# Kernel tuning notes

Hardware: AMD Instinct MI355X
Metric: run time of the kernel (lower is better)

## Reference

```python
import jax, jax.numpy as jnp
import numpy as np

OUT = 7          # pooled output size
SR = 2           # sampling_ratio
STRIDES = (32, 16, 8, 4)          # coarse -> fine, matches feat0..feat3
ANCHORS = (512, 256, 128, 64)     # anchor sizes, large -> small


def _interp_1d(c, size):
    # torchvision roi_align bilinear edge handling (aligned=False)
    valid = (c >= -1.0) & (c <= size)
    cc = jnp.maximum(c, 0.0)
    lo_f = jnp.floor(cc)
    at_edge = lo_f >= size - 1
    lo = jnp.where(at_edge, size - 1.0, lo_f)
    hi = jnp.where(at_edge, size - 1.0, lo_f + 1.0)
    frac = jnp.where(at_edge, 0.0, cc - lo_f)
    return lo.astype(jnp.int32), hi.astype(jnp.int32), frac, valid


def _roi_align(feat, rois, scale):
    # feat: [B,C,H,W], rois: [N,5] = (batch_id, x1, y1, x2, y2)
    B, C, H, W = feat.shape
    N = rois.shape[0]
    b = rois[:, 0].astype(jnp.int32)
    x1, y1, x2, y2 = (rois[:, i] * scale for i in (1, 2, 3, 4))
    roi_w = jnp.maximum(x2 - x1, 1.0)
    roi_h = jnp.maximum(y2 - y1, 1.0)
    bin_h = roi_h / OUT
    bin_w = roi_w / OUT
    off = (jnp.arange(SR) + 0.5) / SR                                 # [SR]
    grid = (jnp.arange(OUT)[:, None] + off[None, :]).reshape(-1)      # [OUT*SR]
    ys = y1[:, None] + grid[None, :] * bin_h[:, None]                 # [N, OUT*SR]
    xs = x1[:, None] + grid[None, :] * bin_w[:, None]
    yl, yh, fy, vy = _interp_1d(ys, H)
    xl, xh, fx, vx = _interp_1d(xs, W)
    ft = jnp.transpose(feat, (0, 2, 3, 1))                            # [B,H,W,C]

    def g(yi, xi):
        return ft[b[:, None, None], yi[:, :, None], xi[:, None, :]]   # [N,Sy,Sx,C]

    wy0 = (1.0 - fy)[:, :, None, None]
    wy1 = fy[:, :, None, None]
    wx0 = (1.0 - fx)[:, None, :, None]
    wx1 = fx[:, None, :, None]
    v = (wy0 * wx0 * g(yl, xl) + wy0 * wx1 * g(yl, xh)
         + wy1 * wx0 * g(yh, xl) + wy1 * wx1 * g(yh, xh))
    v = v * (vy[:, :, None] & vx[:, None, :])[..., None].astype(v.dtype)
    v = v.reshape(N, OUT, SR, OUT, SR, C).mean(axis=(2, 4))           # avg sampling grid
    return jnp.transpose(v, (0, 3, 1, 2))                             # [N,C,OUT,OUT]


def _forward(feats, bboxes):
    B, R, _ = bboxes.shape
    ids = jnp.repeat(jnp.arange(B, dtype=bboxes.dtype), R)[:, None]
    rois = jnp.concatenate([ids, bboxes.reshape(B * R, 4)], axis=-1)  # [N,5]
    areas = (rois[:, 4] - rois[:, 2]) * (rois[:, 3] - rois[:, 1])
    # thresholds from _generate_split_areas: ((min(a_i)+max(a_{i+1}))/2)^2
    thr = [((ANCHORS[i] + ANCHORS[i + 1]) / 2.0) ** 2 for i in range(len(ANCHORS) - 1)]
    levels = sum((areas < t).astype(jnp.int32) for t in thr)          # 0 = coarsest level
    out = jnp.zeros((B * R, feats[0].shape[1], OUT, OUT), dtype=feats[0].dtype)
    for lvl, (feat, stride) in enumerate(zip(feats, STRIDES)):
        pooled = _roi_align(feat, rois, 1.0 / stride)
        out = out + jnp.where((levels == lvl)[:, None, None, None], pooled, 0.0)
    return out


def setup_inputs() -> dict:
    key = jax.random.key(0)
    ks = jax.random.split(key, 8)
    B, C, R, IMG = 2, 256, 512, 1024
    inp = {}
    for i, stride in enumerate(STRIDES):
        hw = IMG // stride
        inp[f"feat{i}"] = jax.random.normal(ks[i], (B, C, hw, hw), dtype=jnp.float32)
    cx = jax.random.uniform(ks[4], (B, R), minval=0.0, maxval=float(IMG))
    cy = jax.random.uniform(ks[5], (B, R), minval=0.0, maxval=float(IMG))
    sz = 16.0 * 2.0 ** (jax.random.uniform(ks[6], (B, R, 2)) * 5.0)   # 16..512 px
    x1 = jnp.clip(cx - sz[..., 0] / 2, 0.0, IMG - 2.0)
    y1 = jnp.clip(cy - sz[..., 1] / 2, 0.0, IMG - 2.0)
    x2 = jnp.clip(cx + sz[..., 0] / 2, x1 + 1.0, float(IMG))
    y2 = jnp.clip(cy + sz[..., 1] / 2, y1 + 1.0, float(IMG))
    inp["bboxes"] = jnp.stack([x1, y1, x2, y2], axis=-1)              # [B,R,4]
    return inp


def reference(feat0, feat1, feat2, feat3, bboxes):
    return _forward([feat0, feat1, feat2, feat3], bboxes)
```

## Files before the change

kernel.cpp:

```cpp
#include <hip/hip_runtime.h>
#include <hip/hip_bf16.h>
#include <cstddef>

__device__ __forceinline__ float bflo(unsigned u) { return __uint_as_float(u << 16); }
__device__ __forceinline__ float bfhi(unsigned u) { return __uint_as_float(u & 0xffff0000u); }

__device__ __forceinline__ unsigned pk(float lo, float hi) {
  __hip_bfloat162 h = __float22bfloat162_rn(float2{lo, hi});
  return *reinterpret_cast<unsigned*>(&h);
}

__device__ __forceinline__ void acc8(const uint4& q, float w, float* acc) {
  acc[0] = fmaf(w, bflo(q.x), acc[0]);
  acc[1] = fmaf(w, bfhi(q.x), acc[1]);
  acc[2] = fmaf(w, bflo(q.y), acc[2]);
  acc[3] = fmaf(w, bfhi(q.y), acc[3]);
  acc[4] = fmaf(w, bflo(q.z), acc[4]);
  acc[5] = fmaf(w, bfhi(q.z), acc[5]);
  acc[6] = fmaf(w, bflo(q.w), acc[6]);
  acc[7] = fmaf(w, bfhi(q.w), acc[7]);
}

__global__ __launch_bounds__(256) void tr_all_kernel(
    const float* __restrict__ f0, const float* __restrict__ f1,
    const float* __restrict__ f2, const float* __restrict__ f3,
    ushort* __restrict__ ws,
    int c0_, int c1_, int c2_, int B,
    size_t o1, size_t o2, size_t o3) {
  __shared__ unsigned tile[16 * 260];
  int bid = blockIdx.x;
  int lvl, lidx; const float* src; size_t off;
  if (bid < c0_)      { lvl = 0; lidx = bid;       src = f0; off = 0; }
  else if (bid < c1_) { lvl = 1; lidx = bid - c0_; src = f1; off = o1; }
  else if (bid < c2_) { lvl = 2; lidx = bid - c1_; src = f2; off = o2; }
  else                { lvl = 3; lidx = bid - c2_; src = f3; off = o3; }
  int H   = 32 << lvl;
  int P   = H * H;
  int Q   = P >> 2;
  int npx = P >> 8;
  int chg = lidx / (B * npx);
  int rem = lidx - chg * (B * npx);
  int b   = rem / npx;
  int pxc = rem - b * npx;

  const float* in = src + (size_t)b * 256 * P;
  int t  = threadIdx.x;
  int l  = t & 63, wv = t >> 6;
  int q  = l >> 4, sub = l & 15;
  size_t lbase = (size_t)q * Q + (size_t)pxc * 64 + sub * 4;
#pragma unroll
  for (int j = 0; j < 4; ++j) {
    int pair = wv * 4 + j;
    int ch   = chg * 32 + pair * 2;
    float4 a = *(const float4*)(in + (size_t)ch * P + lbase);
    float4 c = *(const float4*)(in + (size_t)(ch + 1) * P + lbase);
    uint4 v;
    v.x = pk(a.x, c.x); v.y = pk(a.y, c.y);
    v.z = pk(a.z, c.z); v.w = pk(a.w, c.w);
    *(uint4*)&tile[pair * 260 + l * 4] = v;
  }
  __syncthreads();

  ushort* outp = ws + off + (size_t)b * P * 256 + chg * 32;
  int cg = t & 3;
  int p0 = t >> 2;
#pragma unroll
  for (int i = 0; i < 4; ++i) {
    int pxi = p0 + 64 * i;
    int qq  = pxi >> 6, s = pxi & 63;
    size_t px = (size_t)qq * Q + (size_t)pxc * 64 + s;
    uint4 g;
    g.x = tile[(cg * 4 + 0) * 260 + pxi];
    g.y = tile[(cg * 4 + 1) * 260 + pxi];
    g.z = tile[(cg * 4 + 2) * 260 + pxi];
    g.w = tile[(cg * 4 + 3) * 260 + pxi];
    *(uint4*)(outp + px * 256 + cg * 8) = g;
  }
}

__device__ __forceinline__ void interp1d(float c, int size, int& lo, int& hi,
                                         float& fr, float& va) {
  va = (c >= -1.0f && c <= (float)size) ? 1.0f : 0.0f;
  float cc  = fmaxf(c, 0.0f);
  float lof = floorf(cc);
  if (lof >= (float)(size - 1)) {
    lo = size - 1; hi = size - 1; fr = 0.0f;
  } else {
    lo = (int)lof; hi = lo + 1; fr = cc - lof;
  }
}

__global__ __launch_bounds__(256) void roi_nhwc_kernel(
    const ushort* __restrict__ ws, const float* __restrict__ bboxes,
    float* __restrict__ out, int R, size_t o1, size_t o2, size_t o3) {
  __shared__ float s_out[256 * 49];
  __shared__ int   s_il[2][14], s_ih[2][14];
  __shared__ float s_fr[2][14], s_va[2][14];

  int roi = blockIdx.x;
  int b   = roi / R;
  const float* bb = bboxes + (size_t)roi * 4;
  float x1 = bb[0], y1 = bb[1], x2 = bb[2], y2 = bb[3];

  float area  = (y2 - y1) * (x2 - x1);
  int   level = (area < 147456.0f) + (area < 36864.0f) + (area < 9216.0f);
  int   H     = 32 << level;
  float scale = 1.0f / (float)(32 >> level);
  size_t off  = (level == 0) ? 0 : (level == 1) ? o1 : (level == 2) ? o2 : o3;
  const ushort* fp = ws + off + (size_t)b * H * H * 256;

  float sx1 = x1 * scale, sy1 = y1 * scale;
  float sx2 = x2 * scale, sy2 = y2 * scale;
  float bin_w = fmaxf(sx2 - sx1, 1.0f) / 7.0f;
  float bin_h = fmaxf(sy2 - sy1, 1.0f) / 7.0f;

  int t = threadIdx.x;
  if (t < 28) {
    int   axis  = (t >= 14) ? 1 : 0;
    int   g     = t - axis * 14;
    float start = axis ? sx1 : sy1;
    float binsz = axis ? bin_w : bin_h;
    float grid  = (float)(g >> 1) + 0.25f + 0.5f * (float)(g & 1);
    int lo, hi; float fr, va;
    interp1d(start + grid * binsz, H, lo, hi, fr, va);
    s_il[axis][g] = lo; s_ih[axis][g] = hi;
    s_fr[axis][g] = fr; s_va[axis][g] = va;
  }
  __syncthreads();

  int hw = t >> 5;
  int ln = t & 31;
  int c8 = ln * 8;

  for (int bin = hw; bin < 49; bin += 8) {
    int oy = bin / 7, ox = bin - oy * 7;
    float acc[8] = {0.f, 0.f, 0.f, 0.f, 0.f, 0.f, 0.f, 0.f};
#pragma unroll
    for (int sy = 0; sy < 2; ++sy) {
#pragma unroll
      for (int sx = 0; sx < 2; ++sx) {
        int gy = oy * 2 + sy, gx = ox * 2 + sx;
        int   yl = s_il[0][gy], yh = s_ih[0][gy];
        int   xl = s_il[1][gx], xh = s_ih[1][gx];
        float fy = s_fr[0][gy], fx = s_fr[1][gx];
        float vv = s_va[0][gy] * s_va[1][gx];
        float w00 = (1.f - fy) * (1.f - fx) * vv;
        float w01 = (1.f - fy) * fx * vv;
        float w10 = fy * (1.f - fx) * vv;
        float w11 = fy * fx * vv;
        uint4 q00 = *(const uint4*)(fp + ((size_t)(yl * H + xl) * 256 + c8));
        uint4 q01 = *(const uint4*)(fp + ((size_t)(yl * H + xh) * 256 + c8));
        uint4 q10 = *(const uint4*)(fp + ((size_t)(yh * H + xl) * 256 + c8));
        uint4 q11 = *(const uint4*)(fp + ((size_t)(yh * H + xh) * 256 + c8));
        acc8(q00, w00, acc);
        acc8(q01, w01, acc);
        acc8(q10, w10, acc);
        acc8(q11, w11, acc);
      }
    }
#pragma unroll
    for (int k = 0; k < 8; ++k) s_out[(c8 + k) * 49 + bin] = acc[k] * 0.25f;
  }
  __syncthreads();

  float4*       o4 = (float4*)(out + (size_t)roi * (256 * 49));
  const float4* s4 = (const float4*)s_out;
  for (int i = t; i < 256 * 49 / 4; i += 256) o4[i] = s4[i];
}

__global__ __launch_bounds__(256) void roi_nchw_kernel(
    const float* __restrict__ f0, const float* __restrict__ f1,
    const float* __restrict__ f2, const float* __restrict__ f3,
    const float* __restrict__ bboxes, float* __restrict__ out, int R) {
  __shared__ float s_out[256 * 49];
  __shared__ int   s_il[2][14], s_ih[2][14];
  __shared__ float s_fr[2][14], s_va[2][14];

  int roi = blockIdx.x;
  int b   = roi / R;
  const float* bb = bboxes + (size_t)roi * 4;
  float x1 = bb[0], y1 = bb[1], x2 = bb[2], y2 = bb[3];
  float area  = (y2 - y1) * (x2 - x1);
  int   level = (area < 147456.0f) + (area < 36864.0f) + (area < 9216.0f);
  int   H     = 32 << level;
  float scale = 1.0f / (float)(32 >> level);
  const float* fp = (level == 0) ? f0 : (level == 1) ? f1
                  : (level == 2) ? f2 : f3;
  fp += (size_t)b * 256 * H * H;

  float sx1 = x1 * scale, sy1 = y1 * scale;
  float sx2 = x2 * scale, sy2 = y2 * scale;
  float bin_w = fmaxf(sx2 - sx1, 1.0f) / 7.0f;
  float bin_h = fmaxf(sy2 - sy1, 1.0f) / 7.0f;

  int t = threadIdx.x;
  if (t < 28) {
    int   axis  = (t >= 14) ? 1 : 0;
    int   g     = t - axis * 14;
    float start = axis ? sx1 : sy1;
    float binsz = axis ? bin_w : bin_h;
    float grid  = (float)(g >> 1) + 0.25f + 0.5f * (float)(g & 1);
    int lo, hi; float fr, va;
    interp1d(start + grid * binsz, H, lo, hi, fr, va);
    s_il[axis][g] = lo; s_ih[axis][g] = hi;
    s_fr[axis][g] = fr; s_va[axis][g] = va;
  }
  __syncthreads();

  int wv = t >> 6, ln = t & 63;
  int c4 = ln * 4;
  size_t chs = (size_t)H * H;

  for (int bin = wv; bin < 49; bin += 4) {
    int oy = bin / 7, ox = bin - oy * 7;
    float a0 = 0.f, a1 = 0.f, a2 = 0.f, a3 = 0.f;
#pragma unroll
    for (int sy = 0; sy < 2; ++sy) {
#pragma unroll
      for (int sx = 0; sx < 2; ++sx) {
        int gy = oy * 2 + sy, gx = ox * 2 + sx;
        int   yl = s_il[0][gy], yh = s_ih[0][gy];
        int   xl = s_il[1][gx], xh = s_ih[1][gx];
        float fy = s_fr[0][gy], fx = s_fr[1][gx];
        float vv = s_va[0][gy] * s_va[1][gx];
        float w00 = (1.f - fy) * (1.f - fx) * vv;
        float w01 = (1.f - fy) * fx * vv;
        float w10 = fy * (1.f - fx) * vv;
        float w11 = fy * fx * vv;
        const float* base = fp + (size_t)c4 * chs;
        size_t i00 = (size_t)yl * H + xl, i01 = (size_t)yl * H + xh;
        size_t i10 = (size_t)yh * H + xl, i11 = (size_t)yh * H + xh;
#pragma unroll
        for (int k = 0; k < 4; ++k) {
          float v = w00 * base[i00 + k * chs] + w01 * base[i01 + k * chs] +
                    w10 * base[i10 + k * chs] + w11 * base[i11 + k * chs];
          if (k == 0) a0 += v; else if (k == 1) a1 += v;
          else if (k == 2) a2 += v; else a3 += v;
        }
      }
    }
    s_out[(c4 + 0) * 49 + bin] = a0 * 0.25f;
    s_out[(c4 + 1) * 49 + bin] = a1 * 0.25f;
    s_out[(c4 + 2) * 49 + bin] = a2 * 0.25f;
    s_out[(c4 + 3) * 49 + bin] = a3 * 0.25f;
  }
  __syncthreads();

  float4*       o4 = (float4*)(out + (size_t)roi * (256 * 49));
  const float4* s4 = (const float4*)s_out;
  for (int i = t; i < 256 * 49 / 4; i += 256) o4[i] = s4[i];
}

extern "C" void kernel_launch(void* const* d_in, const int* in_sizes, int n_in,
                              void* d_out, int out_size, void* d_ws, size_t ws_size,
                              hipStream_t stream) {
  const float* f[4];
  for (int i = 0; i < 4; ++i) f[i] = (const float*)d_in[i];
  const float* bb  = (const float*)d_in[4];
  float*       out = (float*)d_out;

  int B = in_sizes[0] / (256 * 32 * 32);
  int N = in_sizes[4] / 4;
  int R = N / B;

  size_t P[4] = {1024, 4096, 16384, 65536};
  size_t o1 = (size_t)B * 256 * P[0];
  size_t o2 = o1 + (size_t)B * 256 * P[1];
  size_t o3 = o2 + (size_t)B * 256 * P[2];
  size_t tot = o3 + (size_t)B * 256 * P[3];

  if (ws_size >= tot * sizeof(ushort)) {
    ushort* ws = (ushort*)d_ws;
    int n0 = B * 8 * (int)(P[0] >> 8);
    int n1 = B * 8 * (int)(P[1] >> 8);
    int n2 = B * 8 * (int)(P[2] >> 8);
    int n3 = B * 8 * (int)(P[3] >> 8);
    int c0 = n0, c1 = c0 + n1, c2 = c1 + n2, ctot = c2 + n3;
    tr_all_kernel<<<ctot, 256, 0, stream>>>(f[0], f[1], f[2], f[3], ws,
                                            c0, c1, c2, B, o1, o2, o3);
    roi_nhwc_kernel<<<N, 256, 0, stream>>>(ws, bb, out, R, o1, o2, o3);
  } else {
    roi_nchw_kernel<<<N, 256, 0, stream>>>(f[0], f[1], f[2], f[3], bb, out, R);
  }
}
```

Baseline: 85.70 us.

## Factor bilinear sampling into merged separable row/column taps to skip duplicate loads

Precomputes, per output bin and axis, up to four unique integer indices with merged weights, combining the two samples' lo/hi taps and folding in the 1/2 averaging factor. The gather loop then visits only unique (row, col) pairs with nonzero weight, so coincident taps are fetched once. This matters for small ROIs, where adjacent samples share pixels. It adds data-dependent branches and divergence inside the gather loop in exchange for fewer global loads.

```diff
diff --git a/kernel.cpp b/kernel.cpp
--- a/kernel.cpp
+++ b/kernel.cpp
@@ -94,8 +94,8 @@
     const ushort* __restrict__ ws, const float* __restrict__ bboxes,
     float* __restrict__ out, int R, size_t o1, size_t o2, size_t o3) {
   __shared__ float s_out[256 * 49];
-  __shared__ int   s_il[2][14], s_ih[2][14];
-  __shared__ float s_fr[2][14], s_va[2][14];
+  __shared__ int   s_ri[2][7][4];
+  __shared__ float s_rw[2][7][4];
 
   int roi = blockIdx.x;
   int b   = roi / R;
@@ -115,16 +115,30 @@
   float bin_h = fmaxf(sy2 - sy1, 1.0f) / 7.0f;
 
   int t = threadIdx.x;
-  if (t < 28) {
-    int   axis  = (t >= 14) ? 1 : 0;
-    int   g     = t - axis * 14;
+  if (t < 14) {
+    int   axis  = t >= 7;
+    int   bn    = t - axis * 7;
     float start = axis ? sx1 : sy1;
     float binsz = axis ? bin_w : bin_h;
-    float grid  = (float)(g >> 1) + 0.25f + 0.5f * (float)(g & 1);
-    int lo, hi; float fr, va;
-    interp1d(start + grid * binsz, H, lo, hi, fr, va);
-    s_il[axis][g] = lo; s_ih[axis][g] = hi;
-    s_fr[axis][g] = fr; s_va[axis][g] = va;
+    int lo0, hi0, lo1, hi1; float f0, f1, v0, v1;
+    interp1d(start + ((float)bn + 0.25f) * binsz, H, lo0, hi0, f0, v0);
+    interp1d(start + ((float)bn + 0.75f) * binsz, H, lo1, hi1, f1, v1);
+    int   idx[4]; float wt[4]; int m = 0;
+    auto add = [&](int id, float w) {
+      for (int k = 0; k < m; ++k)
+        if (idx[k] == id) { wt[k] += w; return; }
+      idx[m] = id; wt[m] = w; ++m;
+    };
+    add(lo0, (1.f - f0) * v0 * 0.5f);
+    add(hi0, f0 * v0 * 0.5f);
+    add(lo1, (1.f - f1) * v1 * 0.5f);
+    add(hi1, f1 * v1 * 0.5f);
+    for (int k = m; k < 4; ++k) { idx[k] = idx[0]; wt[k] = 0.f; }
+#pragma unroll
+    for (int k = 0; k < 4; ++k) {
+      s_ri[axis][bn][k] = idx[k];
+      s_rw[axis][bn][k] = wt[k];
+    }
   }
   __syncthreads();
 
@@ -133,33 +147,23 @@
   int c8 = ln * 8;
 
   for (int bin = hw; bin < 49; bin += 8) {
-    int oy = bin / 7, ox = bin - oy * 7;
+    int by = bin / 7, bx = bin - by * 7;
     float acc[8] = {0.f, 0.f, 0.f, 0.f, 0.f, 0.f, 0.f, 0.f};
 #pragma unroll
-    for (int sy = 0; sy < 2; ++sy) {
-#pragma unroll
-      for (int sx = 0; sx < 2; ++sx) {
-        int gy = oy * 2 + sy, gx = ox * 2 + sx;
-        int   yl = s_il[0][gy], yh = s_ih[0][gy];
-        int   xl = s_il[1][gx], xh = s_ih[1][gx];
-        float fy = s_fr[0][gy], fx = s_fr[1][gx];
-        float vv = s_va[0][gy] * s_va[1][gx];
-        float w00 = (1.f - fy) * (1.f - fx) * vv;
-        float w01 = (1.f - fy) * fx * vv;
-        float w10 = fy * (1.f - fx) * vv;
-        float w11 = fy * fx * vv;
-        uint4 q00 = *(const uint4*)(fp + ((size_t)(yl * H + xl) * 256 + c8));
-        uint4 q01 = *(const uint4*)(fp + ((size_t)(yl * H + xh) * 256 + c8));
-        uint4 q10 = *(const uint4*)(fp + ((size_t)(yh * H + xl) * 256 + c8));
-        uint4 q11 = *(const uint4*)(fp + ((size_t)(yh * H + xh) * 256 + c8));
-        acc8(q00, w00, acc);
-        acc8(q01, w01, acc);
-        acc8(q10, w10, acc);
-        acc8(q11, w11, acc);
+    for (int i = 0; i < 4; ++i) {
+      float wy = s_rw[0][by][i];
+      if (wy == 0.f) continue;
+      const ushort* rowp = fp + (size_t)(s_ri[0][by][i] * H) * 256 + c8;
+#pragma unroll
+      for (int j = 0; j < 4; ++j) {
+        float wx = s_rw[1][bx][j];
+        if (wx == 0.f) continue;
+        uint4 q = *(const uint4*)(rowp + (size_t)s_ri[1][bx][j] * 256);
+        acc8(q, wy * wx, acc);
       }
     }
 #pragma unroll
-    for (int k = 0; k < 8; ++k) s_out[(c8 + k) * 49 + bin] = acc[k] * 0.25f;
+    for (int k = 0; k < 8; ++k) s_out[(c8 + k) * 49 + bin] = acc[k];
   }
   __syncthreads();
 
```

Result: slower. 126.7 us (+47.8%).
